# Kernel optimization log

Hardware: AMD Instinct MI355X
Metric: run time of the kernel (lower is better)

## Reference

```python
import jax, jax.numpy as jnp
import numpy as np

N_Q = 8          # number of residual quantizer stages
N_CODES = 1024   # 2 ** (75 // N_q + 1)
D = 128
GAMMA = 0.99


def setup_inputs() -> dict:
    key = jax.random.key(0)
    k1, k2, k3, k4 = jax.random.split(key, 4)
    data_object = jax.random.normal(k1, (16, D, 2048), dtype=jnp.float32)
    weights = jax.random.normal(k2, (N_Q, N_CODES, D), dtype=jnp.float32)
    # EMA cluster-size buffer; scale so most codes are 'alive' (>= 2)
    N_i = jax.random.uniform(k3, (N_Q, N_CODES), dtype=jnp.float32) * 100.0
    m_i = jax.random.normal(k4, (N_Q, N_CODES, D), dtype=jnp.float32)
    return {"data_object": data_object, "weights": weights, "N_i": N_i, "m_i": m_i}


def reference(data_object, weights, N_i, m_i):
    b, d, s = data_object.shape
    y = jnp.transpose(data_object, (0, 2, 1))  # [b, s, D]
    residual = y
    cur_y = jnp.zeros_like(y)
    all_idx, new_Ni, new_mi, new_W = [], [], [], []
    key = jax.random.key(42)
    one_m_g = 1.0 - GAMMA
    for i in range(N_Q):
        W = weights[i]  # [N, D]
        # squared euclidean distances: ||y||^2 + ||W||^2 - 2 y.W^T  -> [b, s, N]
        dist = ((residual ** 2).sum(-1)[..., None]
                + (W ** 2).sum(-1)[None, None, :]
                - 2.0 * jnp.einsum('bsd,nd->bsn', residual, W))
        idx = jnp.argmin(dist, axis=-1)          # [b, s]
        Q = W[idx]                               # gather  [b, s, D]
        cur_y = cur_y + Q
        flat_idx = idx.reshape(-1)               # [b*s]
        flat_res = residual.reshape(-1, d)       # [b*s, D]
        # fused scatter-reduce replacing the torch per-code mask loop
        counts = jax.ops.segment_sum(jnp.ones(flat_idx.shape, jnp.float32),
                                     flat_idx, num_segments=N_CODES)
        sums = jax.ops.segment_sum(flat_res, flat_idx, num_segments=N_CODES)
        Ni_new = N_i[i] * GAMMA + counts * one_m_g
        mi_new = m_i[i] * GAMMA + sums * one_m_g
        w_new = mi_new / jnp.clip(Ni_new, 1e-8)[:, None]
        # dead-code replacement with random residual vectors
        dead = Ni_new < 2.0
        rid = jax.random.randint(jax.random.fold_in(key, i), (N_CODES,),
                                 0, flat_res.shape[0])
        w_new = jnp.where(dead[:, None], flat_res[rid], w_new)
        all_idx.append(idx)
        new_Ni.append(Ni_new)
        new_mi.append(mi_new)
        new_W.append(w_new)
        residual = residual - Q
    cur_y_t = jnp.transpose(cur_y, (0, 2, 1))  # [b, D, s]
    # straight-through estimator
    logits = data_object + jax.lax.stop_gradient(cur_y_t - data_object)
    commitment_loss = jnp.mean((jax.lax.stop_gradient(cur_y_t) - data_object) ** 2)
    indices = jnp.stack(all_idx, axis=0)  # [N_q, b, s]
    return (logits, commitment_loss, indices,
            jnp.stack(new_Ni), jnp.stack(new_mi), jnp.stack(new_W))
```

## Files before the change

kernel.cpp:

```cpp
#include <hip/hip_runtime.h>
#include <hip/hip_bf16.h>

#define NQ 8
#define NC 1024
#define DD 128
#define BB 16
#define SS 2048
#define RR (BB * SS)
#define GAMMA_F 0.99f
#define TAU 0.03f

typedef __attribute__((ext_vector_type(8))) short bf16x8;
typedef __attribute__((ext_vector_type(4))) float f32x4;

typedef __attribute__((address_space(3))) void lds_void;
typedef const __attribute__((address_space(1))) void g1_void;
__device__ __forceinline__ void gload16(const void* g, void* l) {
  __builtin_amdgcn_global_load_lds((g1_void*)g, (lds_void*)l, 16, 0, 0);
}

__device__ __forceinline__ ushort f2bf(float x) {
  __hip_bfloat16 b = __float2bfloat16(x);
  return *reinterpret_cast<ushort*>(&b);
}
__device__ __forceinline__ float bf2f(ushort u) {
  unsigned v = ((unsigned)u) << 16;
  return *reinterpret_cast<float*>(&v);
}

__device__ __forceinline__ int swz(int r) {
  return ((r & 7) << 2) | ((r >> 3) & 1);
}

__global__ __launch_bounds__(256) void k_transpose_in(
    const float* __restrict__ data, float* __restrict__ res)
{
  __shared__ float tile[32][33];
  int b = blockIdx.z;
  int s0 = blockIdx.x << 5, d0 = blockIdx.y << 5;
  int tx = threadIdx.x, ty = threadIdx.y;
  #pragma unroll
  for (int r = 0; r < 32; r += 8)
    tile[ty + r][tx] = data[((size_t)b * DD + d0 + ty + r) * SS + s0 + tx];
  __syncthreads();
  #pragma unroll
  for (int r = 0; r < 32; r += 8)
    res[((size_t)b * SS + s0 + ty + r) * DD + d0 + tx] = tile[tx][ty + r];
}

__global__ void k_wsq(const float* __restrict__ W, float* __restrict__ wsq)
{
  int c = blockIdx.x * blockDim.x + threadIdx.x;
  if (c >= NQ * NC) return;
  const float4* p = reinterpret_cast<const float4*>(W + (size_t)c * DD);
  float s = 0.f;
  #pragma unroll 8
  for (int k = 0; k < DD / 4; ++k) {
    float4 v = p[k];
    s += v.x * v.x + v.y * v.y + v.z * v.z + v.w * v.w;
  }
  wsq[c] = s;
}

__global__ __launch_bounds__(256) void k_split(
    const float* __restrict__ src, ushort* __restrict__ dst)
{
  int fi = blockIdx.x * 256 + threadIdx.x;
  const float4* sp = reinterpret_cast<const float4*>(src) + (size_t)fi * 2;
  float4 a = sp[0], b = sp[1];
  ushort4 h0, h1, l0, l1;
  h0.x = f2bf(a.x); l0.x = f2bf(a.x - bf2f(h0.x));
  h0.y = f2bf(a.y); l0.y = f2bf(a.y - bf2f(h0.y));
  h0.z = f2bf(a.z); l0.z = f2bf(a.z - bf2f(h0.z));
  h0.w = f2bf(a.w); l0.w = f2bf(a.w - bf2f(h0.w));
  h1.x = f2bf(b.x); l1.x = f2bf(b.x - bf2f(h1.x));
  h1.y = f2bf(b.y); l1.y = f2bf(b.y - bf2f(h1.y));
  h1.z = f2bf(b.z); l1.z = f2bf(b.z - bf2f(h1.z));
  h1.w = f2bf(b.w); l1.w = f2bf(b.w - bf2f(h1.w));
  ushort4* dp = reinterpret_cast<ushort4*>(dst + (size_t)fi * 16);
  dp[0] = h0; dp[1] = h1; dp[2] = l0; dp[3] = l1;
}

__global__ __launch_bounds__(512, 2) void k_argmin(
    const ushort* __restrict__ res_hl, const ushort* __restrict__ w_hl,
    const float* __restrict__ wsq,
    int* __restrict__ idxw, float* __restrict__ idxf,
    int* __restrict__ count, int* __restrict__ fb_count,
    int* __restrict__ fb_list, int stage)
{
  __shared__ bf16x8 S[8192];
  __shared__ float Lm1[2][128], Lm2[2][128];
  __shared__ int   Li1[2][128];

  const int t = threadIdx.x;
  const int l = t & 63;
  const int w = t >> 6;
  const int wm = w >> 1;
  const int wn = w & 1;
  const int row0 = blockIdx.x * 128;
  const int l15 = l & 15, kg = l >> 4;
  const float* wsqs = wsq + stage * NC;

  #pragma unroll
  for (int it = 0; it < 8; ++it) {
    int fi = it * 512 + t;
    int r = fi >> 5, sc = fi & 31;
    gload16(res_hl + ((size_t)(row0 + r) * 32 + (sc ^ swz(r))) * 8, &S[fi]);
  }
  #pragma unroll
  for (int it = 0; it < 8; ++it) {
    int fi = it * 512 + t;
    int cr = fi >> 5, sc = fi & 31;
    gload16(w_hl + ((size_t)(stage * NC + cr) * 32 + (sc ^ swz(cr))) * 8, &S[4096 + fi]);
  }
  asm volatile("s_waitcnt vmcnt(8)" ::: "memory");
  __builtin_amdgcn_sched_barrier(0);
  __builtin_amdgcn_s_barrier();

  bf16x8 ah[2][4], al[2][4];
  #pragma unroll
  for (int mf = 0; mf < 2; ++mf)
    #pragma unroll
    for (int ks = 0; ks < 4; ++ks) {
      int r = wm * 32 + mf * 16 + l15;
      int ch = ks * 8 + kg * 2;
      ah[mf][ks] = S[r * 32 + (ch ^ swz(r))];
      al[mf][ks] = S[r * 32 + ((ch + 1) ^ swz(r))];
    }
  asm volatile("s_waitcnt lgkmcnt(0)" ::: "memory");
  __builtin_amdgcn_sched_barrier(0);
  __builtin_amdgcn_s_barrier();

  #pragma unroll
  for (int it = 0; it < 8; ++it) {
    int fi = it * 512 + t;
    int cr = fi >> 5, sc = fi & 31;
    gload16(w_hl + ((size_t)(stage * NC + 128 + cr) * 32 + (sc ^ swz(cr))) * 8, &S[fi]);
  }

  float m1[2][4], m2[2][4];
  int i1[2][4];
  #pragma unroll
  for (int mf = 0; mf < 2; ++mf)
    #pragma unroll
    for (int rg = 0; rg < 4; ++rg) { m1[mf][rg] = 3.4e38f; m2[mf][rg] = 3.4e38f; i1[mf][rg] = 0; }

  for (int ct = 0; ct < 8; ++ct) {
    if (ct < 7) asm volatile("s_waitcnt vmcnt(8)" ::: "memory");
    else        asm volatile("s_waitcnt vmcnt(0)" ::: "memory");
    __builtin_amdgcn_sched_barrier(0);
    __builtin_amdgcn_s_barrier();

    const bf16x8* Bb = &S[((ct + 1) & 1) ? 4096 : 0];

    f32x4 zero = {0.f, 0.f, 0.f, 0.f};
    f32x4 acc[2][4];
    #pragma unroll
    for (int mf = 0; mf < 2; ++mf)
      #pragma unroll
      for (int nf = 0; nf < 4; ++nf) acc[mf][nf] = zero;

    #pragma unroll
    for (int ks = 0; ks < 4; ++ks) {
      const int ch = ks * 8 + kg * 2;
      #pragma unroll
      for (int nf = 0; nf < 4; ++nf) {
        int cr = wn * 64 + nf * 16 + l15;
        bf16x8 bh = Bb[cr * 32 + (ch ^ swz(cr))];
        bf16x8 bl = Bb[cr * 32 + ((ch + 1) ^ swz(cr))];
        #pragma unroll
        for (int mf = 0; mf < 2; ++mf) {
          f32x4 cc = acc[mf][nf];
          cc = __builtin_amdgcn_mfma_f32_16x16x32_bf16(ah[mf][ks], bh, cc, 0, 0, 0);
          cc = __builtin_amdgcn_mfma_f32_16x16x32_bf16(al[mf][ks], bh, cc, 0, 0, 0);
          cc = __builtin_amdgcn_mfma_f32_16x16x32_bf16(ah[mf][ks], bl, cc, 0, 0, 0);
          acc[mf][nf] = cc;
        }
      }
    }

    #pragma unroll
    for (int nf = 0; nf < 4; ++nf) {
      int code = ct * 128 + wn * 64 + nf * 16 + l15;
      float sq = wsqs[code];
      #pragma unroll
      for (int mf = 0; mf < 2; ++mf)
        #pragma unroll
        for (int rg = 0; rg < 4; ++rg) {
          float s = fmaf(-2.f, acc[mf][nf][rg], sq);
          if (s < m1[mf][rg]) { m2[mf][rg] = m1[mf][rg]; m1[mf][rg] = s; i1[mf][rg] = code; }
          else if (s < m2[mf][rg]) m2[mf][rg] = s;
        }
    }

    __builtin_amdgcn_sched_barrier(0);
    __builtin_amdgcn_s_barrier();
    if (ct + 2 < 8) {
      bf16x8* dst = &S[((ct + 1) & 1) ? 4096 : 0];
      #pragma unroll
      for (int it = 0; it < 8; ++it) {
        int fi = it * 512 + t;
        int cr = fi >> 5, sc = fi & 31;
        gload16(w_hl + ((size_t)(stage * NC + (ct + 2) * 128 + cr) * 32 + (sc ^ swz(cr))) * 8,
                &dst[fi]);
      }
    }
  }

  #pragma unroll
  for (int mk = 1; mk <= 8; mk <<= 1) {
    #pragma unroll
    for (int mf = 0; mf < 2; ++mf)
      #pragma unroll
      for (int rg = 0; rg < 4; ++rg) {
        float om1 = __shfl_xor(m1[mf][rg], mk);
        int   oi  = __shfl_xor(i1[mf][rg], mk);
        float om2 = __shfl_xor(m2[mf][rg], mk);
        bool bwin = (om1 < m1[mf][rg]) || (om1 == m1[mf][rg] && oi < i1[mf][rg]);
        float lose = bwin ? m1[mf][rg] : om1;
        m2[mf][rg] = fminf(fminf(m2[mf][rg], om2), lose);
        if (bwin) { m1[mf][rg] = om1; i1[mf][rg] = oi; }
      }
  }
  if (l15 == 0) {
    #pragma unroll
    for (int mf = 0; mf < 2; ++mf)
      #pragma unroll
      for (int rg = 0; rg < 4; ++rg) {
        int rl = wm * 32 + mf * 16 + kg * 4 + rg;
        Lm1[wn][rl] = m1[mf][rg];
        Lm2[wn][rl] = m2[mf][rg];
        Li1[wn][rl] = i1[mf][rg];
      }
  }
  __syncthreads();

  if (t < 128) {
    float a1 = Lm1[0][t], a2 = Lm2[0][t];
    int ai = Li1[0][t];
    float b1 = Lm1[1][t], b2 = Lm2[1][t];
    int bi = Li1[1][t];
    bool bwin = (b1 < a1) || (b1 == a1 && bi < ai);
    float lose = bwin ? a1 : b1;
    float gm1 = bwin ? b1 : a1;
    int gi = bwin ? bi : ai;
    float gm2 = fminf(fminf(a2, b2), lose);
    int row = row0 + t;
    if (gm2 - gm1 > TAU) {
      idxw[row] = gi;
      idxf[row] = (float)gi;
      atomicAdd(&count[gi], 1);
    } else {
      int p = atomicAdd(fb_count, 1);
      fb_list[p] = row;
    }
  }
}

__global__ __launch_bounds__(256) void k_fallback(
    const float* __restrict__ res, const float* __restrict__ W,
    const float* __restrict__ wsq, const int* __restrict__ fb_count,
    const int* __restrict__ fb_list,
    int* __restrict__ idxw, float* __restrict__ idxf,
    int* __restrict__ count, int stage)
{
  __shared__ float rr[128];
  __shared__ float sv[256];
  __shared__ int   si[256];
  int n = *fb_count;
  int t = threadIdx.x;
  for (int b = blockIdx.x; b < n; b += gridDim.x) {
    int row = fb_list[b];
    __syncthreads();
    if (t < 128) rr[t] = res[(size_t)row * DD + t];
    __syncthreads();
    float bm = 3.4e38f; int bi = 0;
    #pragma unroll
    for (int j = 0; j < 4; ++j) {
      int c = t + j * 256;
      const float4* wp = reinterpret_cast<const float4*>(W + ((size_t)stage * NC + c) * DD);
      float dot = 0.f;
      #pragma unroll 8
      for (int k = 0; k < 32; ++k) {
        float4 wv = wp[k];
        dot = fmaf(rr[4 * k + 0], wv.x, dot);
        dot = fmaf(rr[4 * k + 1], wv.y, dot);
        dot = fmaf(rr[4 * k + 2], wv.z, dot);
        dot = fmaf(rr[4 * k + 3], wv.w, dot);
      }
      float s = fmaf(-2.f, dot, wsq[stage * NC + c]);
      if (s < bm || (s == bm && c < bi)) { bm = s; bi = c; }
    }
    sv[t] = bm; si[t] = bi;
    __syncthreads();
    for (int sft = 128; sft > 0; sft >>= 1) {
      if (t < sft) {
        float ov = sv[t + sft]; int oi = si[t + sft];
        if (ov < sv[t] || (ov == sv[t] && oi < si[t])) { sv[t] = ov; si[t] = oi; }
      }
      __syncthreads();
    }
    if (t == 0) {
      int win = si[0];
      idxw[row] = win;
      idxf[row] = (float)win;
      atomicAdd(&count[win], 1);
    }
  }
}

__global__ __launch_bounds__(1024) void k_scan(
    int* __restrict__ count, int* __restrict__ offs, int* __restrict__ pos)
{
  __shared__ int sc[1024];
  int t = threadIdx.x;
  sc[t] = count[t];
  __syncthreads();
  for (int off = 1; off < 1024; off <<= 1) {
    int v = (t >= off) ? sc[t - off] : 0;
    __syncthreads();
    sc[t] += v;
    __syncthreads();
  }
  offs[t + 1] = sc[t];
  if (t == 0) { offs[0] = 0; count[1024] = 0; }
  pos[t] = 0;
  count[t] = 0;
}

__global__ __launch_bounds__(256) void k_scatter(
    const int* __restrict__ idxw, const int* __restrict__ offs,
    int* __restrict__ pos, int* __restrict__ rows_sorted)
{
  int r = blockIdx.x * 256 + threadIdx.x;
  int c = idxw[r];
  int slot = offs[c] + atomicAdd(&pos[c], 1);
  rows_sorted[slot] = r;
}

__device__ __forceinline__ unsigned rotl32(unsigned v, int r) { return (v << r) | (v >> (32 - r)); }

__device__ void threefry2x32(unsigned ks0, unsigned ks1, unsigned x0, unsigned x1,
                             unsigned& o0, unsigned& o1)
{
  unsigned ks2 = ks0 ^ ks1 ^ 0x1BD11BDAu;
  x0 += ks0; x1 += ks1;
  x0 += x1; x1 = rotl32(x1, 13); x1 ^= x0;
  x0 += x1; x1 = rotl32(x1, 15); x1 ^= x0;
  x0 += x1; x1 = rotl32(x1, 26); x1 ^= x0;
  x0 += x1; x1 = rotl32(x1, 6);  x1 ^= x0;
  x0 += ks1; x1 += ks2 + 1u;
  x0 += x1; x1 = rotl32(x1, 17); x1 ^= x0;
  x0 += x1; x1 = rotl32(x1, 29); x1 ^= x0;
  x0 += x1; x1 = rotl32(x1, 16); x1 ^= x0;
  x0 += x1; x1 = rotl32(x1, 24); x1 ^= x0;
  x0 += ks2; x1 += ks0 + 2u;
  x0 += x1; x1 = rotl32(x1, 13); x1 ^= x0;
  x0 += x1; x1 = rotl32(x1, 15); x1 ^= x0;
  x0 += x1; x1 = rotl32(x1, 26); x1 ^= x0;
  x0 += x1; x1 = rotl32(x1, 6);  x1 ^= x0;
  x0 += ks0; x1 += ks1 + 3u;
  x0 += x1; x1 = rotl32(x1, 17); x1 ^= x0;
  x0 += x1; x1 = rotl32(x1, 29); x1 ^= x0;
  x0 += x1; x1 = rotl32(x1, 16); x1 ^= x0;
  x0 += x1; x1 = rotl32(x1, 24); x1 ^= x0;
  x0 += ks1; x1 += ks2 + 4u;
  x0 += x1; x1 = rotl32(x1, 13); x1 ^= x0;
  x0 += x1; x1 = rotl32(x1, 15); x1 ^= x0;
  x0 += x1; x1 = rotl32(x1, 26); x1 ^= x0;
  x0 += x1; x1 = rotl32(x1, 6);  x1 ^= x0;
  x0 += ks2; x1 += ks0 + 5u;
  o0 = x0; o1 = x1;
}

__global__ __launch_bounds__(1024) void k_finalize(
    const float* __restrict__ Ni_in, const float* __restrict__ mi_in,
    const int* __restrict__ count, const int* __restrict__ offs,
    const int* __restrict__ rows_sorted, const float* __restrict__ res_cur,
    float* __restrict__ outNi, float* __restrict__ outmi, float* __restrict__ outW,
    int stage)
{
  __shared__ float red[8][128];
  const float ONEMG = (float)(1.0 - 0.99);
  int c = blockIdx.x;
  int t = threadIdx.x;
  int d = t & 127;
  int jw = t >> 7;
  int cnt = count[c];
  int base = offs[c];
  const int* rs = rows_sorted + base;

  float sum = 0.f;
  int j = jw;
  for (; j + 24 < cnt; j += 32) {
    int r0 = rs[j];
    int r1 = rs[j + 8];
    int r2 = rs[j + 16];
    int r3 = rs[j + 24];
    float v0 = res_cur[(size_t)r0 * DD + d];
    float v1 = res_cur[(size_t)r1 * DD + d];
    float v2 = res_cur[(size_t)r2 * DD + d];
    float v3 = res_cur[(size_t)r3 * DD + d];
    sum += v0 + v1 + v2 + v3;
  }
  for (; j < cnt; j += 8)
    sum += res_cur[(size_t)rs[j] * DD + d];

  red[jw][d] = sum;
  __syncthreads();

  if (jw == 0) {
    float s = red[0][d] + red[1][d] + red[2][d] + red[3][d]
            + red[4][d] + red[5][d] + red[6][d] + red[7][d];
    float ni = Ni_in[stage * NC + c] * GAMMA_F + (float)cnt * ONEMG;
    float mm = mi_in[((size_t)stage * NC + c) * DD + d] * GAMMA_F + s * ONEMG;
    float w = mm / fmaxf(ni, 1e-8f);
    if (ni < 2.0f) {
      unsigned K0, K1, a0, a1, b0, b1, o0, o1;
      threefry2x32(0u, 42u, 0u, (unsigned)stage, K0, K1);
      threefry2x32(K0, K1, 0u, 2u, a0, a1);
      threefry2x32(K0, K1, 1u, 3u, b0, b1);
      unsigned bits;
      if (c < 512) { threefry2x32(a1, b1, (unsigned)c, (unsigned)(c + 512), o0, o1); bits = o0; }
      else         { threefry2x32(a1, b1, (unsigned)(c - 512), (unsigned)c, o0, o1); bits = o1; }
      int rid = (int)(bits & 32767u);
      w = res_cur[(size_t)rid * DD + d];
    }
    if (d == 0) outNi[stage * NC + c] = ni;
    size_t o = ((size_t)stage * NC + c) * DD + d;
    outmi[o] = mm;
    outW[o] = w;
  }
}

__global__ __launch_bounds__(256) void k_update(
    float* __restrict__ res, const float* __restrict__ W,
    const int* __restrict__ idx, ushort* __restrict__ res_hl, int stage)
{
  int row = blockIdx.x * 8 + (threadIdx.x >> 5);
  int d4 = threadIdx.x & 31;
  int id = idx[row];
  float4 r = reinterpret_cast<const float4*>(res + (size_t)row * DD)[d4];
  float4 q = reinterpret_cast<const float4*>(W + ((size_t)stage * NC + id) * DD)[d4];
  float4 o;
  o.x = r.x - q.x; o.y = r.y - q.y; o.z = r.z - q.z; o.w = r.w - q.w;
  reinterpret_cast<float4*>(res + (size_t)row * DD)[d4] = o;
  ushort4 hi, lo;
  hi.x = f2bf(o.x); lo.x = f2bf(o.x - bf2f(hi.x));
  hi.y = f2bf(o.y); lo.y = f2bf(o.y - bf2f(hi.y));
  hi.z = f2bf(o.z); lo.z = f2bf(o.z - bf2f(hi.z));
  hi.w = f2bf(o.w); lo.w = f2bf(o.w - bf2f(hi.w));
  size_t g = ((size_t)row * 16 + (d4 >> 1)) * 2;
  *reinterpret_cast<ushort4*>(res_hl + g * 8 + (d4 & 1) * 4) = hi;
  *reinterpret_cast<ushort4*>(res_hl + (g + 1) * 8 + (d4 & 1) * 4) = lo;
}

__global__ __launch_bounds__(256) void k_final(
    const float* __restrict__ data, const float* __restrict__ res,
    float* __restrict__ logits, float* __restrict__ partials)
{
  __shared__ float tile[32][33];
  __shared__ float wsum[4];
  int b = blockIdx.z, s0 = blockIdx.x << 5, d0 = blockIdx.y << 5;
  int tx = threadIdx.x, ty = threadIdx.y;
  #pragma unroll
  for (int r = 0; r < 32; r += 8)
    tile[ty + r][tx] = res[((size_t)b * SS + s0 + ty + r) * DD + d0 + tx];
  __syncthreads();
  float l = 0.f;
  #pragma unroll
  for (int r = 0; r < 32; r += 8) {
    int dv = d0 + ty + r, s = s0 + tx;
    size_t o = ((size_t)b * DD + dv) * SS + s;
    float rv = tile[tx][ty + r];
    logits[o] = data[o] - rv;
    l = fmaf(rv, rv, l);
  }
  #pragma unroll
  for (int m = 1; m < 64; m <<= 1) l += __shfl_xor(l, m);
  int lin = ty * 32 + tx;
  if ((lin & 63) == 0) wsum[lin >> 6] = l;
  __syncthreads();
  if (lin == 0) {
    int bl = (blockIdx.z * gridDim.y + blockIdx.y) * gridDim.x + blockIdx.x;
    partials[bl] = wsum[0] + wsum[1] + wsum[2] + wsum[3];
  }
}

__global__ __launch_bounds__(1024) void k_loss_reduce(
    const float* __restrict__ partials, float* __restrict__ loss)
{
  __shared__ float ws[16];
  int t = threadIdx.x;
  float s = partials[t] + partials[t + 1024] + partials[t + 2048] + partials[t + 3072];
  #pragma unroll
  for (int m = 1; m < 64; m <<= 1) s += __shfl_xor(s, m);
  if ((t & 63) == 0) ws[t >> 6] = s;
  __syncthreads();
  if (t < 16) {
    float v = ws[t];
    #pragma unroll
    for (int m = 1; m < 16; m <<= 1) v += __shfl_xor(v, m);
    if (t == 0) loss[0] = v * (1.0f / 4194304.0f);
  }
}

extern "C" void kernel_launch(void* const* d_in, const int* in_sizes, int n_in,
                              void* d_out, int out_size, void* d_ws, size_t ws_size,
                              hipStream_t stream)
{
  (void)in_sizes; (void)n_in; (void)out_size; (void)ws_size;
  const float* data = (const float*)d_in[0];
  const float* W    = (const float*)d_in[1];
  const float* Ni   = (const float*)d_in[2];
  const float* mi   = (const float*)d_in[3];

  float* out        = (float*)d_out;
  float* out_logits = out;
  float* out_loss   = out + (size_t)BB * DD * SS;
  float* out_idx    = out_loss + 1;
  float* out_Ni     = out_idx + (size_t)NQ * RR;
  float* out_mi     = out_Ni + (size_t)NQ * NC;
  float* out_W      = out_mi + (size_t)NQ * NC * DD;

  char* wp = (char*)d_ws;
  float*  resA        = (float*)wp;   wp += (size_t)RR * DD * 4;
  ushort* res_hl      = (ushort*)wp;  wp += (size_t)RR * DD * 4;
  ushort* w_hl        = (ushort*)wp;  wp += (size_t)NQ * NC * DD * 4;
  float*  wsq         = (float*)wp;   wp += (size_t)NQ * NC * 4;
  int*    idxw        = (int*)wp;     wp += (size_t)RR * 4;
  int*    fb_list     = (int*)wp;     wp += (size_t)RR * 4;
  int*    rows_sorted = (int*)wp;     wp += (size_t)RR * 4;
  int*    count       = (int*)wp;     wp += (size_t)1025 * 4;
  int*    fb_count    = count + 1024;
  int*    pos         = (int*)wp;     wp += (size_t)NC * 4;
  int*    offs        = (int*)wp;     wp += (size_t)(NC + 1) * 4;
  float*  partials    = (float*)wp;   wp += (size_t)4096 * 4;

  k_transpose_in<<<dim3(SS / 32, DD / 32, BB), dim3(32, 8), 0, stream>>>(data, resA);
  k_split<<<RR * 16 / 256, 256, 0, stream>>>(resA, res_hl);
  k_wsq<<<(NQ * NC + 255) / 256, 256, 0, stream>>>(W, wsq);
  k_split<<<NQ * NC * 16 / 256, 256, 0, stream>>>(W, w_hl);
  hipMemsetAsync(count, 0, 1025 * sizeof(int), stream);

  for (int i = 0; i < NQ; ++i) {
    k_argmin<<<RR / 128, 512, 0, stream>>>(res_hl, w_hl, wsq, idxw,
                                           out_idx + (size_t)i * RR,
                                           count, fb_count, fb_list, i);
    k_fallback<<<512, 256, 0, stream>>>(resA, W, wsq, fb_count, fb_list,
                                        idxw, out_idx + (size_t)i * RR, count, i);
    k_scan<<<1, 1024, 0, stream>>>(count, offs, pos);
    k_scatter<<<RR / 256, 256, 0, stream>>>(idxw, offs, pos, rows_sorted);
    k_finalize<<<NC, 1024, 0, stream>>>(Ni, mi, count, offs, rows_sorted, resA,
                                        out_Ni, out_mi, out_W, i);
    k_update<<<RR / 8, 256, 0, stream>>>(resA, W, idxw, res_hl, i);
  }

  k_final<<<dim3(SS / 32, DD / 32, BB), dim3(32, 8), 0, stream>>>(data, resA, out_logits, partials);
  k_loss_reduce<<<1, 1024, 0, stream>>>(partials, out_loss);
}
```

Baseline: 783.6 us.

## Shrink argmin tile to 64 rows and load residual fragments directly to registers

The argmin kernel now processes 64 rows per block with 4 code-waves per row group, and codebook tiles drop to 64 codes. This halves LDS use and cuts accumulator registers so launch bounds can request 4 blocks per CU. Residual fragments are read straight from global memory into registers instead of being staged through LDS. In exchange each block reloads the full codebook for half as many rows, doubling codebook traffic, and there are twice as many loop iterations and barriers. finalize also derives counts from offs, presumably because k_scan may reset count.

```diff
diff --git a/kernel.cpp b/kernel.cpp
--- a/kernel.cpp
+++ b/kernel.cpp
@@ -81,61 +81,50 @@
   dp[0] = h0; dp[1] = h1; dp[2] = l0; dp[3] = l1;
 }
 
-__global__ __launch_bounds__(512, 2) void k_argmin(
+__global__ __launch_bounds__(512, 4) void k_argmin(
     const ushort* __restrict__ res_hl, const ushort* __restrict__ w_hl,
     const float* __restrict__ wsq,
     int* __restrict__ idxw, float* __restrict__ idxf,
     int* __restrict__ count, int* __restrict__ fb_count,
     int* __restrict__ fb_list, int stage)
 {
-  __shared__ bf16x8 S[8192];
-  __shared__ float Lm1[2][128], Lm2[2][128];
-  __shared__ int   Li1[2][128];
+  __shared__ bf16x8 Bs[2][2048];
+  __shared__ float Lm1[4][64], Lm2[4][64];
+  __shared__ int   Li1[4][64];
 
   const int t = threadIdx.x;
   const int l = t & 63;
   const int w = t >> 6;
-  const int wm = w >> 1;
-  const int wn = w & 1;
-  const int row0 = blockIdx.x * 128;
+  const int wm = w >> 2;
+  const int wn = w & 3;
+  const int row0 = blockIdx.x * 64;
   const int l15 = l & 15, kg = l >> 4;
   const float* wsqs = wsq + stage * NC;
 
-  #pragma unroll
-  for (int it = 0; it < 8; ++it) {
-    int fi = it * 512 + t;
-    int r = fi >> 5, sc = fi & 31;
-    gload16(res_hl + ((size_t)(row0 + r) * 32 + (sc ^ swz(r))) * 8, &S[fi]);
-  }
-  #pragma unroll
-  for (int it = 0; it < 8; ++it) {
+  bf16x8 ah[2][4], al[2][4];
+  #pragma unroll
+  for (int mf = 0; mf < 2; ++mf) {
+    int r = row0 + wm * 32 + mf * 16 + l15;
+    const bf16x8* rowp = reinterpret_cast<const bf16x8*>(res_hl + (size_t)r * 256);
+    #pragma unroll
+    for (int ks = 0; ks < 4; ++ks) {
+      int ch = ks * 8 + kg * 2;
+      ah[mf][ks] = rowp[ch];
+      al[mf][ks] = rowp[ch + 1];
+    }
+  }
+
+  #pragma unroll
+  for (int it = 0; it < 4; ++it) {
     int fi = it * 512 + t;
     int cr = fi >> 5, sc = fi & 31;
-    gload16(w_hl + ((size_t)(stage * NC + cr) * 32 + (sc ^ swz(cr))) * 8, &S[4096 + fi]);
-  }
-  asm volatile("s_waitcnt vmcnt(8)" ::: "memory");
-  __builtin_amdgcn_sched_barrier(0);
-  __builtin_amdgcn_s_barrier();
-
-  bf16x8 ah[2][4], al[2][4];
-  #pragma unroll
-  for (int mf = 0; mf < 2; ++mf)
-    #pragma unroll
-    for (int ks = 0; ks < 4; ++ks) {
-      int r = wm * 32 + mf * 16 + l15;
-      int ch = ks * 8 + kg * 2;
-      ah[mf][ks] = S[r * 32 + (ch ^ swz(r))];
-      al[mf][ks] = S[r * 32 + ((ch + 1) ^ swz(r))];
-    }
-  asm volatile("s_waitcnt lgkmcnt(0)" ::: "memory");
-  __builtin_amdgcn_sched_barrier(0);
-  __builtin_amdgcn_s_barrier();
-
-  #pragma unroll
-  for (int it = 0; it < 8; ++it) {
+    gload16(w_hl + ((size_t)(stage * NC + cr) * 32 + (sc ^ swz(cr))) * 8, &Bs[0][fi]);
+  }
+  #pragma unroll
+  for (int it = 0; it < 4; ++it) {
     int fi = it * 512 + t;
     int cr = fi >> 5, sc = fi & 31;
-    gload16(w_hl + ((size_t)(stage * NC + 128 + cr) * 32 + (sc ^ swz(cr))) * 8, &S[fi]);
+    gload16(w_hl + ((size_t)(stage * NC + 64 + cr) * 32 + (sc ^ swz(cr))) * 8, &Bs[1][fi]);
   }
 
   float m1[2][4], m2[2][4];
@@ -145,49 +134,42 @@
     #pragma unroll
     for (int rg = 0; rg < 4; ++rg) { m1[mf][rg] = 3.4e38f; m2[mf][rg] = 3.4e38f; i1[mf][rg] = 0; }
 
-  for (int ct = 0; ct < 8; ++ct) {
-    if (ct < 7) asm volatile("s_waitcnt vmcnt(8)" ::: "memory");
-    else        asm volatile("s_waitcnt vmcnt(0)" ::: "memory");
+  for (int ct = 0; ct < 16; ++ct) {
+    if (ct < 15) asm volatile("s_waitcnt vmcnt(4)" ::: "memory");
+    else         asm volatile("s_waitcnt vmcnt(0)" ::: "memory");
     __builtin_amdgcn_sched_barrier(0);
     __builtin_amdgcn_s_barrier();
 
-    const bf16x8* Bb = &S[((ct + 1) & 1) ? 4096 : 0];
+    const bf16x8* Bb = Bs[ct & 1];
+    const int cr = wn * 16 + l15;
 
     f32x4 zero = {0.f, 0.f, 0.f, 0.f};
-    f32x4 acc[2][4];
-    #pragma unroll
-    for (int mf = 0; mf < 2; ++mf)
-      #pragma unroll
-      for (int nf = 0; nf < 4; ++nf) acc[mf][nf] = zero;
+    f32x4 acc[2];
+    acc[0] = zero; acc[1] = zero;
 
     #pragma unroll
     for (int ks = 0; ks < 4; ++ks) {
       const int ch = ks * 8 + kg * 2;
+      bf16x8 bh = Bb[cr * 32 + (ch ^ swz(cr))];
+      bf16x8 bl = Bb[cr * 32 + ((ch + 1) ^ swz(cr))];
       #pragma unroll
-      for (int nf = 0; nf < 4; ++nf) {
-        int cr = wn * 64 + nf * 16 + l15;
-        bf16x8 bh = Bb[cr * 32 + (ch ^ swz(cr))];
-        bf16x8 bl = Bb[cr * 32 + ((ch + 1) ^ swz(cr))];
-        #pragma unroll
-        for (int mf = 0; mf < 2; ++mf) {
-          f32x4 cc = acc[mf][nf];
-          cc = __builtin_amdgcn_mfma_f32_16x16x32_bf16(ah[mf][ks], bh, cc, 0, 0, 0);
-          cc = __builtin_amdgcn_mfma_f32_16x16x32_bf16(al[mf][ks], bh, cc, 0, 0, 0);
-          cc = __builtin_amdgcn_mfma_f32_16x16x32_bf16(ah[mf][ks], bl, cc, 0, 0, 0);
-          acc[mf][nf] = cc;
-        }
+      for (int mf = 0; mf < 2; ++mf) {
+        f32x4 cc = acc[mf];
+        cc = __builtin_amdgcn_mfma_f32_16x16x32_bf16(ah[mf][ks], bh, cc, 0, 0, 0);
+        cc = __builtin_amdgcn_mfma_f32_16x16x32_bf16(al[mf][ks], bh, cc, 0, 0, 0);
+        cc = __builtin_amdgcn_mfma_f32_16x16x32_bf16(ah[mf][ks], bl, cc, 0, 0, 0);
+        acc[mf] = cc;
       }
     }
 
-    #pragma unroll
-    for (int nf = 0; nf < 4; ++nf) {
-      int code = ct * 128 + wn * 64 + nf * 16 + l15;
+    {
+      int code = ct * 64 + wn * 16 + l15;
       float sq = wsqs[code];
       #pragma unroll
       for (int mf = 0; mf < 2; ++mf)
         #pragma unroll
         for (int rg = 0; rg < 4; ++rg) {
-          float s = fmaf(-2.f, acc[mf][nf][rg], sq);
+          float s = fmaf(-2.f, acc[mf][rg], sq);
           if (s < m1[mf][rg]) { m2[mf][rg] = m1[mf][rg]; m1[mf][rg] = s; i1[mf][rg] = code; }
           else if (s < m2[mf][rg]) m2[mf][rg] = s;
         }
@@ -195,13 +177,13 @@
 
     __builtin_amdgcn_sched_barrier(0);
     __builtin_amdgcn_s_barrier();
-    if (ct + 2 < 8) {
-      bf16x8* dst = &S[((ct + 1) & 1) ? 4096 : 0];
+    if (ct + 2 < 16) {
+      bf16x8* dst = Bs[ct & 1];
       #pragma unroll
-      for (int it = 0; it < 8; ++it) {
+      for (int it = 0; it < 4; ++it) {
         int fi = it * 512 + t;
-        int cr = fi >> 5, sc = fi & 31;
-        gload16(w_hl + ((size_t)(stage * NC + (ct + 2) * 128 + cr) * 32 + (sc ^ swz(cr))) * 8,
+        int cr2 = fi >> 5, sc = fi & 31;
+        gload16(w_hl + ((size_t)(stage * NC + (ct + 2) * 64 + cr2) * 32 + (sc ^ swz(cr2))) * 8,
                 &dst[fi]);
       }
     }
@@ -235,16 +217,18 @@
   }
   __syncthreads();
 
-  if (t < 128) {
-    float a1 = Lm1[0][t], a2 = Lm2[0][t];
-    int ai = Li1[0][t];
-    float b1 = Lm1[1][t], b2 = Lm2[1][t];
-    int bi = Li1[1][t];
-    bool bwin = (b1 < a1) || (b1 == a1 && bi < ai);
-    float lose = bwin ? a1 : b1;
-    float gm1 = bwin ? b1 : a1;
-    int gi = bwin ? bi : ai;
-    float gm2 = fminf(fminf(a2, b2), lose);
+  if (t < 64) {
+    float gm1 = Lm1[0][t], gm2 = Lm2[0][t];
+    int gi = Li1[0][t];
+    #pragma unroll
+    for (int q = 1; q < 4; ++q) {
+      float b1 = Lm1[q][t], b2 = Lm2[q][t];
+      int bi = Li1[q][t];
+      bool bwin = (b1 < gm1) || (b1 == gm1 && bi < gi);
+      float lose = bwin ? gm1 : b1;
+      gm2 = fminf(fminf(gm2, b2), lose);
+      if (bwin) { gm1 = b1; gi = bi; }
+    }
     int row = row0 + t;
     if (gm2 - gm1 > TAU) {
       idxw[row] = gi;
@@ -375,8 +359,8 @@
 
 __global__ __launch_bounds__(1024) void k_finalize(
     const float* __restrict__ Ni_in, const float* __restrict__ mi_in,
-    const int* __restrict__ count, const int* __restrict__ offs,
-    const int* __restrict__ rows_sorted, const float* __restrict__ res_cur,
+    const int* __restrict__ offs, const int* __restrict__ rows_sorted,
+    const float* __restrict__ res_cur,
     float* __restrict__ outNi, float* __restrict__ outmi, float* __restrict__ outW,
     int stage)
 {
@@ -386,8 +370,8 @@
   int t = threadIdx.x;
   int d = t & 127;
   int jw = t >> 7;
-  int cnt = count[c];
   int base = offs[c];
+  int cnt = offs[c + 1] - base;
   const int* rs = rows_sorted + base;
 
   float sum = 0.f;
@@ -544,14 +528,14 @@
   hipMemsetAsync(count, 0, 1025 * sizeof(int), stream);
 
   for (int i = 0; i < NQ; ++i) {
-    k_argmin<<<RR / 128, 512, 0, stream>>>(res_hl, w_hl, wsq, idxw,
-                                           out_idx + (size_t)i * RR,
-                                           count, fb_count, fb_list, i);
+    k_argmin<<<RR / 64, 512, 0, stream>>>(res_hl, w_hl, wsq, idxw,
+                                          out_idx + (size_t)i * RR,
+                                          count, fb_count, fb_list, i);
     k_fallback<<<512, 256, 0, stream>>>(resA, W, wsq, fb_count, fb_list,
                                         idxw, out_idx + (size_t)i * RR, count, i);
     k_scan<<<1, 1024, 0, stream>>>(count, offs, pos);
     k_scatter<<<RR / 256, 256, 0, stream>>>(idxw, offs, pos, rows_sorted);
-    k_finalize<<<NC, 1024, 0, stream>>>(Ni, mi, count, offs, rows_sorted, resA,
+    k_finalize<<<NC, 1024, 0, stream>>>(Ni, mi, offs, rows_sorted, resA,
                                         out_Ni, out_mi, out_W, i);
     k_update<<<RR / 8, 256, 0, stream>>>(resA, W, idxw, res_hl, i);
   }
```

Result: slower. 927.4 us (+18.3%).
